# Performance work log

Hardware: AMD Instinct MI355X
Metric: run time of the kernel (lower is better)

Reference implementation:

```python
import jax, jax.numpy as jnp
import numpy as np

BITS = 4
GROUP = 128
M, K, N = 16, 4096, 11008


def setup_inputs() -> dict:
    key = jax.random.key(0)
    k1, k2, k3 = jax.random.split(key, 3)
    A = jax.random.normal(k1, (M, K), dtype=jnp.float16)
    # packed 4-bit weights: 2 nibbles per byte, stored as int32 holding 0..255
    qweight = jax.random.randint(k2, (N, K * BITS // 8), 0, 256, dtype=jnp.int32)
    # small positive-ish scales like real GPTQ checkpoints
    scales = (jax.random.normal(k3, (N, K // GROUP)) * 0.01 + 0.02).astype(jnp.float16)
    zeros = jnp.zeros((N, K // GROUP), dtype=jnp.float16)
    bias = jnp.zeros((N,), dtype=jnp.float16)
    return {"A": A, "qweight": qweight, "scales": scales, "zeros": zeros, "bias": bias}


def _dequant(qweight, scales, zeros):
    # qweight: (N, K//2) packed; element idx -> byte idx//2, low nibble if idx even
    low = qweight & 0xF
    high = (qweight >> 4) & 0xF
    w_int = jnp.stack([low, high], axis=-1).reshape(qweight.shape[0], -1)  # (N, K)
    # per-group dequant with 'original' zeros: W = (q - z) * s
    s = jnp.repeat(scales, GROUP, axis=1)  # (N, K)
    z = jnp.repeat(zeros, GROUP, axis=1)   # (N, K)
    return (w_int.astype(jnp.float16) - z) * s


def reference(A, qweight, scales, zeros, bias):
    W = _dequant(qweight, scales, zeros)           # (N, K) fp16
    return jnp.matmul(A, W.T) + bias               # (M, N) fp16
```

## Files before the change

### kernel.cpp

```cpp
#include <hip/hip_runtime.h>

#define KK 4096
#define NN 11008
#define NGRP 32
#define KW 2048
#define WS_RS_OFF 131072
#define WS_SZ_OFF 139264

using short8  = __attribute__((ext_vector_type(8))) short;
using float4v = __attribute__((ext_vector_type(4))) float;

static __device__ __forceinline__ unsigned int pack_bf16(float lo, float hi) {
    unsigned int ul = __builtin_bit_cast(unsigned int, lo);
    unsigned int uh = __builtin_bit_cast(unsigned int, hi);
    ul = (ul + 0x7FFFu + ((ul >> 16) & 1u)) >> 16;
    uh = (uh + 0x7FFFu + ((uh >> 16) & 1u)) & 0xFFFF0000u;
    return ul | uh;
}
static __device__ __forceinline__ float bf16val(float f) {
    unsigned int u = __builtin_bit_cast(unsigned int, f);
    u = (u + 0x7FFFu + ((u >> 16) & 1u)) & 0xFFFF0000u;
    return __builtin_bit_cast(float, u);
}

__global__ __launch_bounds__(256) void prep_kernel(
    const float* __restrict__ A, const float* __restrict__ scales,
    const float* __restrict__ zeros, unsigned short* __restrict__ wsA,
    float* __restrict__ rowsum, float* __restrict__ SZ)
{
    const int b = blockIdx.x, t = threadIdx.x;
    if (b < 32) {
        const int tid = b * 256 + t;
        const int c = tid >> 6, l = tid & 63;
        const float* src = A + (size_t)(l & 15) * KK + c * 32 + (l >> 4) * 8;
        float4v x0 = *(const float4v*)src;
        float4v x1 = *(const float4v*)(src + 4);
        union { short8 s8; unsigned int u[4]; } p;
        p.u[0] = pack_bf16(x0[0], x0[1]);
        p.u[1] = pack_bf16(x0[2], x0[3]);
        p.u[2] = pack_bf16(x1[0], x1[1]);
        p.u[3] = pack_bf16(x1[2], x1[3]);
        *(short8*)(wsA + (size_t)tid * 8) = p.s8;
    } else if (b < 64) {
        const int sid = (b - 32) * 16 + (t >> 4);
        const int m = sid >> 5, g = sid & 31, j = t & 15;
        const float* p = A + (size_t)m * KK + g * 128 + j * 8;
        float4v x0 = *(const float4v*)p;
        float4v x1 = *(const float4v*)(p + 4);
        float sum = bf16val(x0[0]) + bf16val(x0[1]) + bf16val(x0[2]) + bf16val(x0[3])
                  + bf16val(x1[0]) + bf16val(x1[1]) + bf16val(x1[2]) + bf16val(x1[3]);
        sum += __shfl_xor(sum, 1, 16);
        sum += __shfl_xor(sum, 2, 16);
        sum += __shfl_xor(sum, 4, 16);
        sum += __shfl_xor(sum, 8, 16);
        if (j == 0) rowsum[sid] = sum;
    } else {
        const int e0 = (b - 64) * 1024 + t * 4;
        float4v s4 = *(const float4v*)(scales + e0);
        float4v z4 = *(const float4v*)(zeros + e0);
        float4v r;
        #pragma unroll
        for (int j = 0; j < 4; ++j) r[j] = s4[j] * (128.0f + z4[j]);
        *(float4v*)(SZ + e0) = r;
    }
}

__global__ __launch_bounds__(256) void init_out_kernel(
    const float* __restrict__ bias, const float* __restrict__ SZ,
    const float* __restrict__ rowsum, float* __restrict__ out)
{
    __shared__ float rs[16][32];
    const int t = threadIdx.x;
    rs[t >> 5][t & 31]       = rowsum[t];
    rs[(t >> 5) + 8][t & 31] = rowsum[t + 256];
    __syncthreads();
    const int n0 = blockIdx.x * 16;
    const int m = t >> 4, nn = t & 15, ng = n0 + nn;
    const float* szr = SZ + (size_t)ng * NGRP;
    float corr = 0.f;
    #pragma unroll
    for (int g = 0; g < 32; ++g)
        corr = __builtin_fmaf(szr[g], rs[m][g], corr);
    out[(size_t)m * NN + ng] = bias[ng] - corr;
}

__global__ __launch_bounds__(256) void qgemm_kernel(
    const int*            __restrict__ qweight,
    const float*          __restrict__ scales,
    const unsigned short* __restrict__ aperm,
    float*                __restrict__ out)
{
    const int nt = blockIdx.x >> 3, slice = blockIdx.x & 7;
    const int n0 = nt * 16;
    const int wid = threadIdx.x >> 6, lane = threadIdx.x & 63;
    const int nl = lane & 15, quad = lane >> 4;
    const int n = n0 + nl;
    const int g = slice * 4 + wid;

    const int* qrow = qweight + (size_t)n * KW + g * 64 + quad * 4;
    const unsigned short* ap = aperm + (size_t)g * 2048 + lane * 8;

    int4   w0 = *(const int4*)(qrow);
    int4   w1 = *(const int4*)(qrow + 16);
    int4   w2 = *(const int4*)(qrow + 32);
    int4   w3 = *(const int4*)(qrow + 48);
    short8 a0 = *(const short8*)(ap);
    short8 a1 = *(const short8*)(ap + 512);
    short8 a2 = *(const short8*)(ap + 1024);
    short8 a3 = *(const short8*)(ap + 1536);
    const float s = scales[n * NGRP + g];

    float4v acc = {0.f, 0.f, 0.f, 0.f};
    int4 wv[4] = {w0, w1, w2, w3};
    short8 av[4] = {a0, a1, a2, a3};
    #pragma unroll
    for (int t = 0; t < 4; ++t) {
        const unsigned int x0 = (unsigned int)wv[t].x, x1 = (unsigned int)wv[t].y;
        const unsigned int x2 = (unsigned int)wv[t].z, x3 = (unsigned int)wv[t].w;
        union { short8 s8; unsigned int u[4]; } bf;
        bf.u[0] = (x0 & 0xFu) | ((x0 << 12) & 0x000F0000u) | 0x43004300u;
        bf.u[1] = (x1 & 0xFu) | ((x1 << 12) & 0x000F0000u) | 0x43004300u;
        bf.u[2] = (x2 & 0xFu) | ((x2 << 12) & 0x000F0000u) | 0x43004300u;
        bf.u[3] = (x3 & 0xFu) | ((x3 << 12) & 0x000F0000u) | 0x43004300u;
        acc = __builtin_amdgcn_mfma_f32_16x16x32_bf16(av[t], bf.s8, acc, 0, 0, 0);
    }

    __shared__ float red[4][16][16];
    #pragma unroll
    for (int r = 0; r < 4; ++r)
        red[wid][quad * 4 + r][nl] = s * acc[r];
    __syncthreads();

    const int t = threadIdx.x;
    const int m = t >> 4, nn = t & 15;
    float val = red[0][m][nn] + red[1][m][nn] + red[2][m][nn] + red[3][m][nn];
    atomicAdd(&out[(size_t)m * NN + n0 + nn], val);
}

extern "C" void kernel_launch(void* const* d_in, const int* in_sizes, int n_in,
                              void* d_out, int out_size, void* d_ws, size_t ws_size,
                              hipStream_t stream) {
    const float* A       = (const float*)d_in[0];
    const int*   qweight = (const int*)d_in[1];
    const float* scales  = (const float*)d_in[2];
    const float* zeros   = (const float*)d_in[3];
    const float* bias    = (const float*)d_in[4];
    float*       out     = (float*)d_out;

    unsigned short* wsA = (unsigned short*)d_ws;
    float* rowsum       = (float*)((char*)d_ws + WS_RS_OFF);
    float* SZ           = (float*)((char*)d_ws + WS_SZ_OFF);

    prep_kernel<<<dim3(408), dim3(256), 0, stream>>>(A, scales, zeros, wsA, rowsum, SZ);
    init_out_kernel<<<dim3(688), dim3(256), 0, stream>>>(bias, SZ, rowsum, out);
    qgemm_kernel<<<dim3(5504), dim3(256), 0, stream>>>(qweight, scales, wsA, out);
}
```

Measured before the change: 144.4 us.

## Fuse zero-point correction and bias into qgemm, drop atomics and init kernel

```diff
diff --git a/kernel.cpp b/kernel.cpp
--- a/kernel.cpp
+++ b/kernel.cpp
@@ -5,7 +5,6 @@
 #define NGRP 32
 #define KW 2048
 #define WS_RS_OFF 131072
-#define WS_SZ_OFF 139264
 
 using short8  = __attribute__((ext_vector_type(8))) short;
 using float4v = __attribute__((ext_vector_type(4))) float;
@@ -24,9 +23,8 @@
 }
 
 __global__ __launch_bounds__(256) void prep_kernel(
-    const float* __restrict__ A, const float* __restrict__ scales,
-    const float* __restrict__ zeros, unsigned short* __restrict__ wsA,
-    float* __restrict__ rowsum, float* __restrict__ SZ)
+    const float* __restrict__ A, unsigned short* __restrict__ wsA,
+    float* __restrict__ rowsum)
 {
     const int b = blockIdx.x, t = threadIdx.x;
     if (b < 32) {
@@ -41,7 +39,7 @@
         p.u[2] = pack_bf16(x1[0], x1[1]);
         p.u[3] = pack_bf16(x1[2], x1[3]);
         *(short8*)(wsA + (size_t)tid * 8) = p.s8;
-    } else if (b < 64) {
+    } else {
         const int sid = (b - 32) * 16 + (t >> 4);
         const int m = sid >> 5, g = sid & 31, j = t & 15;
         const float* p = A + (size_t)m * KK + g * 128 + j * 8;
@@ -54,87 +52,107 @@
         sum += __shfl_xor(sum, 4, 16);
         sum += __shfl_xor(sum, 8, 16);
         if (j == 0) rowsum[sid] = sum;
-    } else {
-        const int e0 = (b - 64) * 1024 + t * 4;
-        float4v s4 = *(const float4v*)(scales + e0);
-        float4v z4 = *(const float4v*)(zeros + e0);
-        float4v r;
-        #pragma unroll
-        for (int j = 0; j < 4; ++j) r[j] = s4[j] * (128.0f + z4[j]);
-        *(float4v*)(SZ + e0) = r;
     }
 }
 
-__global__ __launch_bounds__(256) void init_out_kernel(
-    const float* __restrict__ bias, const float* __restrict__ SZ,
-    const float* __restrict__ rowsum, float* __restrict__ out)
-{
-    __shared__ float rs[16][32];
-    const int t = threadIdx.x;
-    rs[t >> 5][t & 31]       = rowsum[t];
-    rs[(t >> 5) + 8][t & 31] = rowsum[t + 256];
-    __syncthreads();
-    const int n0 = blockIdx.x * 16;
-    const int m = t >> 4, nn = t & 15, ng = n0 + nn;
-    const float* szr = SZ + (size_t)ng * NGRP;
-    float corr = 0.f;
-    #pragma unroll
-    for (int g = 0; g < 32; ++g)
-        corr = __builtin_fmaf(szr[g], rs[m][g], corr);
-    out[(size_t)m * NN + ng] = bias[ng] - corr;
-}
-
-__global__ __launch_bounds__(256) void qgemm_kernel(
+__global__ __launch_bounds__(512, 4) void qgemm_kernel(
     const int*            __restrict__ qweight,
     const float*          __restrict__ scales,
+    const float*          __restrict__ zeros,
+    const float*          __restrict__ bias,
     const unsigned short* __restrict__ aperm,
+    const float*          __restrict__ rowsum,
     float*                __restrict__ out)
 {
-    const int nt = blockIdx.x >> 3, slice = blockIdx.x & 7;
-    const int n0 = nt * 16;
-    const int wid = threadIdx.x >> 6, lane = threadIdx.x & 63;
+    __shared__ float red[8][16][16];
+    __shared__ float szs[32][17];
+    __shared__ float rss[16][33];
+
+    const int t = threadIdx.x;
+    const int n0 = blockIdx.x * 16;
+    const int wid = t >> 6, lane = t & 63;
     const int nl = lane & 15, quad = lane >> 4;
     const int n = n0 + nl;
-    const int g = slice * 4 + wid;
+    const int g0 = wid * 4;
 
-    const int* qrow = qweight + (size_t)n * KW + g * 64 + quad * 4;
-    const unsigned short* ap = aperm + (size_t)g * 2048 + lane * 8;
+    const int* qrow = qweight + (size_t)n * KW + g0 * 64 + quad * 4;
+    const unsigned short* ap = aperm + (size_t)g0 * 2048 + (size_t)lane * 8;
 
-    int4   w0 = *(const int4*)(qrow);
-    int4   w1 = *(const int4*)(qrow + 16);
-    int4   w2 = *(const int4*)(qrow + 32);
-    int4   w3 = *(const int4*)(qrow + 48);
-    short8 a0 = *(const short8*)(ap);
-    short8 a1 = *(const short8*)(ap + 512);
-    short8 a2 = *(const short8*)(ap + 1024);
-    short8 a3 = *(const short8*)(ap + 1536);
-    const float s = scales[n * NGRP + g];
+    const int sg = t & 31, sn = t >> 5;
+    const float sv = scales[(size_t)(n0 + sn) * NGRP + sg];
+    const float zv = zeros[(size_t)(n0 + sn) * NGRP + sg];
+    const float rv = rowsum[t];
 
-    float4v acc = {0.f, 0.f, 0.f, 0.f};
-    int4 wv[4] = {w0, w1, w2, w3};
-    short8 av[4] = {a0, a1, a2, a3};
+    int4 qw[4][4];
     #pragma unroll
-    for (int t = 0; t < 4; ++t) {
-        const unsigned int x0 = (unsigned int)wv[t].x, x1 = (unsigned int)wv[t].y;
-        const unsigned int x2 = (unsigned int)wv[t].z, x3 = (unsigned int)wv[t].w;
-        union { short8 s8; unsigned int u[4]; } bf;
-        bf.u[0] = (x0 & 0xFu) | ((x0 << 12) & 0x000F0000u) | 0x43004300u;
-        bf.u[1] = (x1 & 0xFu) | ((x1 << 12) & 0x000F0000u) | 0x43004300u;
-        bf.u[2] = (x2 & 0xFu) | ((x2 << 12) & 0x000F0000u) | 0x43004300u;
-        bf.u[3] = (x3 & 0xFu) | ((x3 << 12) & 0x000F0000u) | 0x43004300u;
-        acc = __builtin_amdgcn_mfma_f32_16x16x32_bf16(av[t], bf.s8, acc, 0, 0, 0);
+    for (int j = 0; j < 4; ++j)
+        #pragma unroll
+        for (int c = 0; c < 4; ++c)
+            qw[j][c] = *(const int4*)(qrow + j * 64 + c * 16);
+
+    float sj[4];
+    #pragma unroll
+    for (int j = 0; j < 4; ++j)
+        sj[j] = scales[(size_t)n * NGRP + g0 + j];
+
+    short8 apA[4], apB[4];
+    #pragma unroll
+    for (int c = 0; c < 4; ++c) apA[c] = *(const short8*)(ap + c * 512);
+    #pragma unroll
+    for (int c = 0; c < 4; ++c) apB[c] = *(const short8*)(ap + 2048 + c * 512);
+
+    szs[sg][sn] = sv * (128.0f + zv);
+    rss[t >> 5][t & 31] = rv;
+
+    float4v tot = {0.f, 0.f, 0.f, 0.f};
+
+#define DEQ_MFMA(J, APV)                                                      \
+    {                                                                         \
+        float4v accg = {0.f, 0.f, 0.f, 0.f};                                  \
+        _Pragma("unroll")                                                     \
+        for (int c = 0; c < 4; ++c) {                                         \
+            const unsigned int x0 = (unsigned int)qw[J][c].x;                 \
+            const unsigned int x1 = (unsigned int)qw[J][c].y;                 \
+            const unsigned int x2 = (unsigned int)qw[J][c].z;                 \
+            const unsigned int x3 = (unsigned int)qw[J][c].w;                 \
+            union { short8 s8; unsigned int u[4]; } bf;      \
+            bf.u[0] = (x0 & 0xFu) | ((x0 << 12) & 0x000F0000u) | 0x43004300u; \
+            bf.u[1] = (x1 & 0xFu) | ((x1 << 12) & 0x000F0000u) | 0x43004300u; \
+            bf.u[2] = (x2 & 0xFu) | ((x2 << 12) & 0x000F0000u) | 0x43004300u; \
+            bf.u[3] = (x3 & 0xFu) | ((x3 << 12) & 0x000F0000u) | 0x43004300u; \
+            accg = __builtin_amdgcn_mfma_f32_16x16x32_bf16(APV[c], bf.s8,     \
+                                                           accg, 0, 0, 0);    \
+        }                                                                     \
+        _Pragma("unroll")                                                     \
+        for (int r = 0; r < 4; ++r) tot[r] += sj[J] * accg[r];                \
     }
 
-    __shared__ float red[4][16][16];
+    DEQ_MFMA(0, apA)
+    #pragma unroll
+    for (int c = 0; c < 4; ++c) apA[c] = *(const short8*)(ap + 2 * 2048 + c * 512);
+    DEQ_MFMA(1, apB)
+    #pragma unroll
+    for (int c = 0; c < 4; ++c) apB[c] = *(const short8*)(ap + 3 * 2048 + c * 512);
+    DEQ_MFMA(2, apA)
+    DEQ_MFMA(3, apB)
+#undef DEQ_MFMA
+
     #pragma unroll
     for (int r = 0; r < 4; ++r)
-        red[wid][quad * 4 + r][nl] = s * acc[r];
+        red[wid][quad * 4 + r][nl] = tot[r];
     __syncthreads();
 
-    const int t = threadIdx.x;
-    const int m = t >> 4, nn = t & 15;
-    float val = red[0][m][nn] + red[1][m][nn] + red[2][m][nn] + red[3][m][nn];
-    atomicAdd(&out[(size_t)m * NN + n0 + nn], val);
+    if (t < 256) {
+        const int m = t >> 4, nn = t & 15;
+        float v = 0.f;
+        #pragma unroll
+        for (int w = 0; w < 8; ++w) v += red[w][m][nn];
+        float corr = 0.f;
+        #pragma unroll
+        for (int g = 0; g < 32; ++g)
+            corr = __builtin_fmaf(szs[g][nn], rss[m][g], corr);
+        out[(size_t)m * NN + n0 + nn] = bias[n0 + nn] + v - corr;
+    }
 }
 
 extern "C" void kernel_launch(void* const* d_in, const int* in_sizes, int n_in,
@@ -149,9 +167,8 @@
 
     unsigned short* wsA = (unsigned short*)d_ws;
     float* rowsum       = (float*)((char*)d_ws + WS_RS_OFF);
-    float* SZ           = (float*)((char*)d_ws + WS_SZ_OFF);
 
-    prep_kernel<<<dim3(408), dim3(256), 0, stream>>>(A, scales, zeros, wsA, rowsum, SZ);
-    init_out_kernel<<<dim3(688), dim3(256), 0, stream>>>(bias, SZ, rowsum, out);
-    qgemm_kernel<<<dim3(5504), dim3(256), 0, stream>>>(qweight, scales, wsA, out);
+    prep_kernel<<<dim3(64), dim3(256), 0, stream>>>(A, wsA, rowsum);
+    qgemm_kernel<<<dim3(688), dim3(512), 0, stream>>>(qweight, scales, zeros, bias,
+                                                      wsA, rowsum, out);
 }
```

After: 145.9 us. About the same (+1.0%).
